# Kernel optimization log

Measured on AMD Instinct MI355X. Metric: run time of the kernel, lower is better.

Reference implementation:

```python
import jax, jax.numpy as jnp
import numpy as np

N = 100000
E = 3200000
H = 4        # heads
C = 8        # hidden_dim per head
G = 512      # number of graphs
F_IN = 128
NEG_SLOPE = 0.2


def glorot(key, shape):
    fan = shape[0] + shape[-1]
    lim = jnp.sqrt(6.0 / fan)
    return jax.random.uniform(key, shape, jnp.float32, -lim, lim)


def setup_inputs() -> dict:
    key = jax.random.key(0)
    ks = jax.random.split(key, 32)
    x = jax.random.normal(ks[0], (N, F_IN), jnp.float32)
    edge_index = jax.random.randint(ks[1], (2, E), 0, N, jnp.int64)
    batch = jnp.sort(jax.random.randint(ks[2], (N,), 0, G, jnp.int64))
    d = {"x": x, "edge_index": edge_index, "batch": batch}
    in_dims = [F_IN, H * C, H * C, H * C]
    for i, din in enumerate(in_dims, start=1):
        d[f"W{i}"] = glorot(ks[3 + 4 * i], (din, H * C))
        d[f"as{i}"] = glorot(ks[4 + 4 * i], (H, C))
        d[f"ad{i}"] = glorot(ks[5 + 4 * i], (H, C))
        d[f"b{i}"] = jnp.zeros((H * C,), jnp.float32)
    d["fc_w"] = glorot(ks[30], (H * C, 1))
    d["fc_b"] = jnp.zeros((1,), jnp.float32)
    return d


def gat_layer(x, src, dst, W, a_src, a_dst, b):
    # x: [N, din]; src/dst: [E'] (with self-loops); returns [N, H*C]
    h = (x @ W).reshape(N, H, C)                         # [N,H,C]
    al_s = jnp.einsum('nhc,hc->nh', h, a_src)            # [N,H]
    al_d = jnp.einsum('nhc,hc->nh', h, a_dst)
    e = jax.nn.leaky_relu(al_s[src] + al_d[dst], NEG_SLOPE)  # [E',H]
    m = jax.ops.segment_max(e, dst, num_segments=N)      # [N,H]
    ee = jnp.exp(e - m[dst])
    denom = jax.ops.segment_sum(ee, dst, num_segments=N) # [N,H]
    alpha = ee / denom[dst]
    msg = alpha[:, :, None] * h[src]                     # [E',H,C]
    out = jax.ops.segment_sum(msg, dst, num_segments=N)  # [N,H,C]
    return out.reshape(N, H * C) + b


def reference(x, edge_index, batch, W1, as1, ad1, b1, W2, as2, ad2, b2,
              W3, as3, ad3, b3, W4, as4, ad4, b4, fc_w, fc_b):
    # PyG GATConv default: add self-loops
    loop = jnp.arange(N, dtype=edge_index.dtype)
    src = jnp.concatenate([edge_index[0], loop])
    dst = jnp.concatenate([edge_index[1], loop])
    h = jax.nn.elu(gat_layer(x, src, dst, W1, as1, ad1, b1))
    h = jax.nn.elu(gat_layer(h, src, dst, W2, as2, ad2, b2))
    h = jax.nn.elu(gat_layer(h, src, dst, W3, as3, ad3, b3))
    h = jax.nn.elu(gat_layer(h, src, dst, W4, as4, ad4, b4))
    # global mean pool over graphs
    sums = jax.ops.segment_sum(h, batch, num_segments=G)          # [G,HC]
    cnts = jax.ops.segment_sum(jnp.ones((N,), h.dtype), batch, num_segments=G)
    pooled = sums / jnp.maximum(cnts, 1.0)[:, None]
    return pooled @ fc_w + fc_b                                   # [G,1]
```

## Files before the change

### kernel.cpp

```cpp
#include <hip/hip_runtime.h>
#include <hip/hip_fp16.h>
#include <math.h>

#define NN 100000
#define NE 3200000
#define NHEAD 4
#define HC 32
#define NG 512
#define EDGES (NE + NN)

#define G1BLKS (NN / 8)

#define BKT_BITS 9
#define BKT_SIZE 512
#define NBKT 196
#define CHUNK1 16384
#define NB1 ((EDGES + CHUNK1 - 1) / CHUNK1)
#define NB1S 204
#define CAP2 18432
#define NBIN2 2048
#define PCHUNK 128

__device__ __forceinline__ float lrelu(float x) { return x > 0.f ? x : 0.2f * x; }
__device__ __forceinline__ int src_quarter(int src) {
    return (src >= 50000) ? ((src >= 75000) ? 3 : 2) : ((src >= 25000) ? 1 : 0);
}

__global__ __launch_bounds__(256) void gemm1(
    const float* __restrict__ x, const float* __restrict__ W1,
    const float* __restrict__ as1, const float* __restrict__ ad1,
    __half* __restrict__ h, float* __restrict__ als, float* __restrict__ ald) {
    __shared__ float Wl[128 * HC];
    __shared__ float xl[8][128];
    int tid = threadIdx.x;
    for (int i = tid; i < 128 * HC; i += 256) Wl[i] = W1[i];
    int n0 = blockIdx.x * 8;
    {
        float4 v = *reinterpret_cast<const float4*>(x + n0 * 128 + tid * 4);
        int idx = tid * 4;
        int r = idx >> 7, c = idx & 127;
        *reinterpret_cast<float4*>(&xl[r][c]) = v;
    }
    __syncthreads();
    int r = tid >> 5, col = tid & 31;
    int n = n0 + r;
    float acc = 0.f;
#pragma unroll
    for (int k = 0; k < 128; ++k) acc = fmaf(xl[r][k], Wl[k * HC + col], acc);
    float s = acc * as1[col];
    float d = acc * ad1[col];
#pragma unroll
    for (int off = 1; off < 8; off <<= 1) {
        s += __shfl_xor(s, off);
        d += __shfl_xor(d, off);
    }
    h[n * HC + col] = __float2half(acc);
    if ((col & 7) == 0) {
        als[n * NHEAD + (col >> 3)] = s;
        ald[n * NHEAD + (col >> 3)] = d;
    }
}

__global__ __launch_bounds__(512) void pass1_hist(const int* __restrict__ ei,
                                                  int* __restrict__ CmatT) {
    __shared__ int hcnt[NBKT];
    for (int i = threadIdx.x; i < NBKT; i += 512) hcnt[i] = 0;
    __syncthreads();
    int base = blockIdx.x * CHUNK1;
    int lim = min(base + CHUNK1, EDGES);
    for (int e = base + threadIdx.x; e < lim; e += 512) {
        int dst = (e < NE) ? ei[NE + e] : (e - NE);
        atomicAdd(&hcnt[dst >> BKT_BITS], 1);
    }
    __syncthreads();
    for (int i = threadIdx.x; i < NBKT; i += 512)
        CmatT[i * NB1S + blockIdx.x] = hcnt[i];
}

__global__ __launch_bounds__(64) void colscan2(int* __restrict__ CmatT,
                                               int* __restrict__ degTot) {
    int k = blockIdx.x;
    int lane = threadIdx.x;
    int* p = CmatT + k * NB1S;
    int i0 = lane * 4;
    int v0 = (i0 + 0 < NB1) ? p[i0 + 0] : 0;
    int v1 = (i0 + 1 < NB1) ? p[i0 + 1] : 0;
    int v2 = (i0 + 2 < NB1) ? p[i0 + 2] : 0;
    int v3 = (i0 + 3 < NB1) ? p[i0 + 3] : 0;
    int e1 = v0, e2 = v0 + v1, e3 = v0 + v1 + v2;
    int tot = e3 + v3;
    int run = tot;
#pragma unroll
    for (int off = 1; off < 64; off <<= 1) {
        int u = __shfl_up(run, off);
        if (lane >= off) run += u;
    }
    int excl = run - tot;
    if (i0 + 0 < NB1) p[i0 + 0] = excl;
    if (i0 + 1 < NB1) p[i0 + 1] = excl + e1;
    if (i0 + 2 < NB1) p[i0 + 2] = excl + e2;
    if (i0 + 3 < NB1) p[i0 + 3] = excl + e3;
    if (lane == 63) degTot[k] = run;
}

__global__ __launch_bounds__(256) void bucket_apex(const int* __restrict__ degTot,
                                                   int* __restrict__ bucketStart) {
    __shared__ int tot[256];
    int k = threadIdx.x;
    int own = (k < NBKT) ? degTot[k] : 0;
    tot[k] = own;
    __syncthreads();
    for (int off = 1; off < 256; off <<= 1) {
        int u = (k >= off) ? tot[k - off] : 0;
        __syncthreads();
        tot[k] += u;
        __syncthreads();
    }
    if (k < NBKT) bucketStart[k] = tot[k] - own;
    if (k == 255) bucketStart[NBKT] = tot[255];
}

__global__ __launch_bounds__(512) void pass1_scatter(const int* __restrict__ ei,
                                                     const int* __restrict__ CmatT,
                                                     const int* __restrict__ bucketStart,
                                                     unsigned int* __restrict__ ebuf) {
    __shared__ int cur[NBKT];
    for (int i = threadIdx.x; i < NBKT; i += 512)
        cur[i] = bucketStart[i] + CmatT[i * NB1S + blockIdx.x];
    __syncthreads();
    int base = blockIdx.x * CHUNK1;
    int lim = min(base + CHUNK1, EDGES);
    for (int e = base + threadIdx.x; e < lim; e += 512) {
        int src, dst;
        if (e < NE) { src = ei[e]; dst = ei[NE + e]; }
        else        { src = dst = e - NE; }
        int pos = atomicAdd(&cur[dst >> BKT_BITS], 1);
        ebuf[pos] = ((unsigned int)(dst & (BKT_SIZE - 1)) << 20) | (unsigned int)src;
    }
}

__global__ __launch_bounds__(1024) void pass2_sort(const unsigned int* __restrict__ ebuf,
                                                   const int* __restrict__ bucketStart,
                                                   int* __restrict__ csrsrc,
                                                   int* __restrict__ rowst) {
    __shared__ int hist[NBIN2];
    __shared__ int pairs[1024];
    __shared__ int staging[CAP2];
    int t = threadIdx.x;
    int k = blockIdx.x;
    int start = bucketStart[k], end = bucketStart[k + 1];
    int count = end - start;
    hist[t] = 0;
    hist[t + 1024] = 0;
    __syncthreads();
    for (int i = start + t; i < end; i += 1024) {
        unsigned int v = ebuf[i];
        int src = (int)(v & 0xFFFFFu);
        atomicAdd(&hist[(int)((v >> 20) << 2) | src_quarter(src)], 1);
    }
    __syncthreads();
    int h0 = hist[2 * t], h1 = hist[2 * t + 1];
    pairs[t] = h0 + h1;
    __syncthreads();
    for (int off = 1; off < 1024; off <<= 1) {
        int u = (t >= off) ? pairs[t - off] : 0;
        __syncthreads();
        pairs[t] += u;
        __syncthreads();
    }
    int e0 = pairs[t] - h0 - h1;
    int e1 = e0 + h0;
    __syncthreads();
    hist[2 * t] = e0;
    hist[2 * t + 1] = e1;
    if ((t & 1) == 0) rowst[k * BKT_SIZE + (t >> 1)] = start + e0;
    __syncthreads();
    for (int i = start + t; i < end; i += 1024) {
        unsigned int v = ebuf[i];
        int src = (int)(v & 0xFFFFFu);
        int pos = atomicAdd(&hist[(int)((v >> 20) << 2) | src_quarter(src)], 1);
        if (pos < CAP2) staging[pos] = src;
    }
    __syncthreads();
    for (int i = t; i < count; i += 1024) csrsrc[start + i] = staging[i];
}

template<bool FUSE>
__global__ __launch_bounds__(256) void agg_layer(
    const int* __restrict__ rowst, const int* __restrict__ csrsrc,
    const float* __restrict__ als, const float* __restrict__ ald,
    const __half* __restrict__ h, const float* __restrict__ bias,
    const float* __restrict__ Wn, const float* __restrict__ asn,
    const float* __restrict__ adn,
    __half* __restrict__ h_out, float* __restrict__ als_out,
    float* __restrict__ ald_out, float* __restrict__ act_out) {
    __shared__ float Wl[HC * HC];
    int tid = threadIdx.x;
    if (FUSE) {
        for (int i = tid; i < HC * HC; i += 256) Wl[i] = Wn[i];
        __syncthreads();
    }
    int g = blockIdx.x * 8 + (tid >> 5);
    int lane = tid & 31;
    int head = lane >> 3;
    int slot = lane & 7;
    float adh = ald[g * NHEAD + head];
    int beg = rowst[g], end = rowst[g + 1];

    float acc[8];
#pragma unroll
    for (int j = 0; j < 8; ++j) acc[j] = 0.f;
    float dsum = 0.f;
    const __half* hL = h + lane;

    for (int c0 = beg; c0 < end; c0 += 16) {
        int eA = c0 + slot;
        int eB = eA + 8;
        int sA = (eA < end) ? __builtin_nontemporal_load(csrsrc + eA) : 0;
        int sB = (eB < end) ? __builtin_nontemporal_load(csrsrc + eB) : 0;
        float pA = __expf(lrelu(als[sA * NHEAD + head] + adh));
        float pB = __expf(lrelu(als[sB * NHEAD + head] + adh));
        pA = (eA < end) ? pA : 0.f;
        pB = (eB < end) ? pB : 0.f;
        dsum += pA + pB;
        int sjA[8], sjB[8];
#pragma unroll
        for (int j = 0; j < 8; ++j) {
            sjA[j] = __shfl(sA, j, 32);
            sjB[j] = __shfl(sB, j, 32);
        }
        __half hvA[8], hvB[8];
#pragma unroll
        for (int j = 0; j < 8; ++j) hvA[j] = hL[sjA[j] * HC];
#pragma unroll
        for (int j = 0; j < 8; ++j) hvB[j] = hL[sjB[j] * HC];
#pragma unroll
        for (int j = 0; j < 8; ++j)
            acc[j] = fmaf(__shfl(pA, (head << 3) | j, 32), __half2float(hvA[j]), acc[j]);
#pragma unroll
        for (int j = 0; j < 8; ++j)
            acc[j] = fmaf(__shfl(pB, (head << 3) | j, 32), __half2float(hvB[j]), acc[j]);
    }
    float a = ((acc[0] + acc[1]) + (acc[2] + acc[3])) +
              ((acc[4] + acc[5]) + (acc[6] + acc[7]));
    dsum += __shfl_xor(dsum, 1, 32);
    dsum += __shfl_xor(dsum, 2, 32);
    dsum += __shfl_xor(dsum, 4, 32);

    float v = a / dsum + bias[lane];
    float av = v > 0.f ? v : (__expf(v) - 1.f);
    if (!FUSE) {
        act_out[g * HC + lane] = av;
        return;
    }
    float hacc = 0.f;
#pragma unroll
    for (int kk = 0; kk < HC; ++kk)
        hacc = fmaf(__shfl(av, kk, 32), Wl[kk * HC + lane], hacc);
    h_out[g * HC + lane] = __float2half(hacc);
    float sv = hacc * asn[lane];
    float dv = hacc * adn[lane];
#pragma unroll
    for (int off = 1; off < 8; off <<= 1) {
        sv += __shfl_xor(sv, off);
        dv += __shfl_xor(dv, off);
    }
    if ((lane & 7) == 0) {
        als_out[g * NHEAD + head] = sv;
        ald_out[g * NHEAD + head] = dv;
    }
}

__global__ void pool_init(float* __restrict__ sums, float* __restrict__ cnt) {
    int i = blockIdx.x * blockDim.x + threadIdx.x;
    if (i < NG * HC) sums[i] = 0.f;
    if (i < NG) cnt[i] = 0.f;
}

__global__ __launch_bounds__(256) void pool_seg(const float* __restrict__ act,
                                                const int* __restrict__ batch,
                                                float* __restrict__ sums,
                                                float* __restrict__ cnt) {
    int grp = blockIdx.x * 8 + (threadIdx.x >> 5);
    int lane = threadIdx.x & 31;
    int n0 = grp * PCHUNK;
    if (n0 >= NN) return;
    int n1 = min(n0 + PCHUNK, NN);
    int curg = batch[n0];
    float acc = 0.f, c = 0.f;
    for (int n = n0; n < n1; ++n) {
        int gg = batch[n];
        if (gg != curg) {
            atomicAdd(&sums[curg * HC + lane], acc);
            if (lane == 0) atomicAdd(&cnt[curg], c);
            acc = 0.f; c = 0.f; curg = gg;
        }
        acc += act[n * HC + lane];
        c += 1.f;
    }
    atomicAdd(&sums[curg * HC + lane], acc);
    if (lane == 0) atomicAdd(&cnt[curg], c);
}

__global__ void fc_out(const float* __restrict__ sums, const float* __restrict__ cnt,
                       const float* __restrict__ fcw, const float* __restrict__ fcb,
                       float* __restrict__ out) {
    int g = blockIdx.x;
    int lane = threadIdx.x;
    float v = (lane < HC) ? sums[g * HC + lane] * fcw[lane] : 0.f;
#pragma unroll
    for (int off = 32; off; off >>= 1) v += __shfl_down(v, off);
    if (lane == 0) out[g] = v / fmaxf(cnt[g], 1.f) + fcb[0];
}

extern "C" void kernel_launch(void* const* d_in, const int* in_sizes, int n_in,
                              void* d_out, int out_size, void* d_ws, size_t ws_size,
                              hipStream_t stream) {
    const float* x     = (const float*)d_in[0];
    const int*   ei    = (const int*)d_in[1];
    const int*   batch = (const int*)d_in[2];
    const float* W[4]   = {(const float*)d_in[3],  (const float*)d_in[7],
                           (const float*)d_in[11], (const float*)d_in[15]};
    const float* asr[4] = {(const float*)d_in[4],  (const float*)d_in[8],
                           (const float*)d_in[12], (const float*)d_in[16]};
    const float* adt[4] = {(const float*)d_in[5],  (const float*)d_in[9],
                           (const float*)d_in[13], (const float*)d_in[17]};
    const float* bb[4]  = {(const float*)d_in[6],  (const float*)d_in[10],
                           (const float*)d_in[14], (const float*)d_in[18]};
    const float* fcw = (const float*)d_in[19];
    const float* fcb = (const float*)d_in[20];
    float* out = (float*)d_out;

    char* ws = (char*)d_ws;
    size_t off = 0;
    auto carve = [&](size_t bytes) {
        void* p = ws + off;
        off += (bytes + 255) & ~size_t(255);
        return p;
    };
    __half* hA   = (__half*)carve(sizeof(__half) * NN * HC);
    __half* hB   = (__half*)carve(sizeof(__half) * NN * HC);
    float* actF  = (float*)carve(sizeof(float) * NN * HC);
    float* alsA  = (float*)carve(sizeof(float) * NN * NHEAD);
    float* aldA  = (float*)carve(sizeof(float) * NN * NHEAD);
    float* alsB  = (float*)carve(sizeof(float) * NN * NHEAD);
    float* aldB  = (float*)carve(sizeof(float) * NN * NHEAD);
    int*   CmatT = (int*)carve(sizeof(int) * NBKT * NB1S);
    int*   degTot= (int*)carve(sizeof(int) * NBKT);
    int*   bkst  = (int*)carve(sizeof(int) * (NBKT + 1));
    unsigned int* ebuf = (unsigned int*)carve(sizeof(unsigned int) * EDGES);
    int*   rowst = (int*)carve(sizeof(int) * NBKT * BKT_SIZE);
    int*   csrsrc= (int*)carve(sizeof(int) * EDGES);
    float* sums  = (float*)carve(sizeof(float) * NG * HC);
    float* cnt   = (float*)carve(sizeof(float) * NG);

    pass1_hist<<<NB1, 512, 0, stream>>>(ei, CmatT);
    colscan2<<<NBKT, 64, 0, stream>>>(CmatT, degTot);
    bucket_apex<<<1, 256, 0, stream>>>(degTot, bkst);
    pass1_scatter<<<NB1, 512, 0, stream>>>(ei, CmatT, bkst, ebuf);
    pass2_sort<<<NBKT, 1024, 0, stream>>>(ebuf, bkst, csrsrc, rowst);

    gemm1<<<G1BLKS, 256, 0, stream>>>(x, W[0], asr[0], adt[0], hA, alsA, aldA);

    agg_layer<true><<<G1BLKS, 256, 0, stream>>>(rowst, csrsrc, alsA, aldA, hA, bb[0],
                                                W[1], asr[1], adt[1],
                                                hB, alsB, aldB, nullptr);
    agg_layer<true><<<G1BLKS, 256, 0, stream>>>(rowst, csrsrc, alsB, aldB, hB, bb[1],
                                                W[2], asr[2], adt[2],
                                                hA, alsA, aldA, nullptr);
    agg_layer<true><<<G1BLKS, 256, 0, stream>>>(rowst, csrsrc, alsA, aldA, hA, bb[2],
                                                W[3], asr[3], adt[3],
                                                hB, alsB, aldB, nullptr);
    agg_layer<false><<<G1BLKS, 256, 0, stream>>>(rowst, csrsrc, alsB, aldB, hB, bb[3],
                                                 nullptr, nullptr, nullptr,
                                                 nullptr, nullptr, nullptr, actF);

    pool_init<<<(NG * HC + 255) / 256, 256, 0, stream>>>(sums, cnt);
    pool_seg<<<((NN + PCHUNK - 1) / PCHUNK + 7) / 8, 256, 0, stream>>>(actF, batch,
                                                                       sums, cnt);
    fc_out<<<NG, 64, 0, stream>>>(sums, cnt, fcw, fcb, out);
}
```

Measured before the change: 473.0 us.

## Split aggregation into four source-quarter passes for cache locality

Each node's CSR row is split into four sub-ranges by source quarter, which the sort already orders by. Aggregation runs as four launches per layer, each gathering only from one quarter of the feature table, so the gathered working set is smaller and more likely to stay in cache. Partial numerators and denominators go through global scratch buffers between launches. The cost is extra launches, extra global reads and writes of the partials, and a loop unrolled over 8 edges instead of 16.

```diff
diff --git a/kernel.cpp b/kernel.cpp
--- a/kernel.cpp
+++ b/kernel.cpp
@@ -142,7 +142,7 @@
 __global__ __launch_bounds__(1024) void pass2_sort(const unsigned int* __restrict__ ebuf,
                                                    const int* __restrict__ bucketStart,
                                                    int* __restrict__ csrsrc,
-                                                   int* __restrict__ rowst) {
+                                                   int* __restrict__ rowst4) {
     __shared__ int hist[NBIN2];
     __shared__ int pairs[1024];
     __shared__ int staging[CAP2];
@@ -173,7 +173,8 @@
     __syncthreads();
     hist[2 * t] = e0;
     hist[2 * t + 1] = e1;
-    if ((t & 1) == 0) rowst[k * BKT_SIZE + (t >> 1)] = start + e0;
+    rowst4[(k << 11) | (2 * t)]     = start + e0;
+    rowst4[(k << 11) | (2 * t + 1)] = start + e1;
     __syncthreads();
     for (int i = start + t; i < end; i += 1024) {
         unsigned int v = ebuf[i];
@@ -185,11 +186,13 @@
     for (int i = t; i < count; i += 1024) csrsrc[start + i] = staging[i];
 }
 
-template<bool FUSE>
-__global__ __launch_bounds__(256) void agg_layer(
-    const int* __restrict__ rowst, const int* __restrict__ csrsrc,
+template<int PHASE, bool FUSE>
+__global__ __launch_bounds__(256) void agg_q(
+    const int* __restrict__ rowst4, const int* __restrict__ csrsrc,
     const float* __restrict__ als, const float* __restrict__ ald,
-    const __half* __restrict__ h, const float* __restrict__ bias,
+    const __half* __restrict__ h, int q,
+    float* __restrict__ accP, float* __restrict__ dsumP,
+    const float* __restrict__ bias,
     const float* __restrict__ Wn, const float* __restrict__ asn,
     const float* __restrict__ adn,
     __half* __restrict__ h_out, float* __restrict__ als_out,
@@ -205,7 +208,7 @@
     int head = lane >> 3;
     int slot = lane & 7;
     float adh = ald[g * NHEAD + head];
-    int beg = rowst[g], end = rowst[g + 1];
+    int beg = rowst4[g * 4 + q], end = rowst4[g * 4 + q + 1];
 
     float acc[8];
 #pragma unroll
@@ -213,33 +216,18 @@
     float dsum = 0.f;
     const __half* hL = h + lane;
 
-    for (int c0 = beg; c0 < end; c0 += 16) {
-        int eA = c0 + slot;
-        int eB = eA + 8;
-        int sA = (eA < end) ? __builtin_nontemporal_load(csrsrc + eA) : 0;
-        int sB = (eB < end) ? __builtin_nontemporal_load(csrsrc + eB) : 0;
-        float pA = __expf(lrelu(als[sA * NHEAD + head] + adh));
-        float pB = __expf(lrelu(als[sB * NHEAD + head] + adh));
-        pA = (eA < end) ? pA : 0.f;
-        pB = (eB < end) ? pB : 0.f;
-        dsum += pA + pB;
-        int sjA[8], sjB[8];
+    for (int c0 = beg; c0 < end; c0 += 8) {
+        int e = c0 + slot;
+        int s = (e < end) ? __builtin_nontemporal_load(csrsrc + e) : 0;
+        float p = __expf(lrelu(als[s * NHEAD + head] + adh));
+        p = (e < end) ? p : 0.f;
+        dsum += p;
 #pragma unroll
         for (int j = 0; j < 8; ++j) {
-            sjA[j] = __shfl(sA, j, 32);
-            sjB[j] = __shfl(sB, j, 32);
+            float pj = __shfl(p, (head << 3) | j, 32);
+            int sj = __shfl(s, j, 32);
+            acc[j] = fmaf(pj, __half2float(hL[sj * HC]), acc[j]);
         }
-        __half hvA[8], hvB[8];
-#pragma unroll
-        for (int j = 0; j < 8; ++j) hvA[j] = hL[sjA[j] * HC];
-#pragma unroll
-        for (int j = 0; j < 8; ++j) hvB[j] = hL[sjB[j] * HC];
-#pragma unroll
-        for (int j = 0; j < 8; ++j)
-            acc[j] = fmaf(__shfl(pA, (head << 3) | j, 32), __half2float(hvA[j]), acc[j]);
-#pragma unroll
-        for (int j = 0; j < 8; ++j)
-            acc[j] = fmaf(__shfl(pB, (head << 3) | j, 32), __half2float(hvB[j]), acc[j]);
     }
     float a = ((acc[0] + acc[1]) + (acc[2] + acc[3])) +
               ((acc[4] + acc[5]) + (acc[6] + acc[7]));
@@ -247,6 +235,23 @@
     dsum += __shfl_xor(dsum, 2, 32);
     dsum += __shfl_xor(dsum, 4, 32);
 
+    if (PHASE == 0) {
+        __builtin_nontemporal_store(a, accP + g * HC + lane);
+        if (slot == 0)
+            __builtin_nontemporal_store(dsum, dsumP + g * NHEAD + head);
+        return;
+    }
+    if (PHASE == 1) {
+        float pa = __builtin_nontemporal_load(accP + g * HC + lane);
+        __builtin_nontemporal_store(a + pa, accP + g * HC + lane);
+        if (slot == 0) {
+            float pd = __builtin_nontemporal_load(dsumP + g * NHEAD + head);
+            __builtin_nontemporal_store(dsum + pd, dsumP + g * NHEAD + head);
+        }
+        return;
+    }
+    a += __builtin_nontemporal_load(accP + g * HC + lane);
+    dsum += __builtin_nontemporal_load(dsumP + g * NHEAD + head);
     float v = a / dsum + bias[lane];
     float av = v > 0.f ? v : (__expf(v) - 1.f);
     if (!FUSE) {
@@ -341,6 +346,8 @@
     __half* hA   = (__half*)carve(sizeof(__half) * NN * HC);
     __half* hB   = (__half*)carve(sizeof(__half) * NN * HC);
     float* actF  = (float*)carve(sizeof(float) * NN * HC);
+    float* accP  = (float*)carve(sizeof(float) * NN * HC);
+    float* dsumP = (float*)carve(sizeof(float) * NN * NHEAD);
     float* alsA  = (float*)carve(sizeof(float) * NN * NHEAD);
     float* aldA  = (float*)carve(sizeof(float) * NN * NHEAD);
     float* alsB  = (float*)carve(sizeof(float) * NN * NHEAD);
@@ -349,7 +356,7 @@
     int*   degTot= (int*)carve(sizeof(int) * NBKT);
     int*   bkst  = (int*)carve(sizeof(int) * (NBKT + 1));
     unsigned int* ebuf = (unsigned int*)carve(sizeof(unsigned int) * EDGES);
-    int*   rowst = (int*)carve(sizeof(int) * NBKT * BKT_SIZE);
+    int*   rowst4= (int*)carve(sizeof(int) * NBKT * NBIN2);
     int*   csrsrc= (int*)carve(sizeof(int) * EDGES);
     float* sums  = (float*)carve(sizeof(float) * NG * HC);
     float* cnt   = (float*)carve(sizeof(float) * NG);
@@ -358,22 +365,37 @@
     colscan2<<<NBKT, 64, 0, stream>>>(CmatT, degTot);
     bucket_apex<<<1, 256, 0, stream>>>(degTot, bkst);
     pass1_scatter<<<NB1, 512, 0, stream>>>(ei, CmatT, bkst, ebuf);
-    pass2_sort<<<NBKT, 1024, 0, stream>>>(ebuf, bkst, csrsrc, rowst);
+    pass2_sort<<<NBKT, 1024, 0, stream>>>(ebuf, bkst, csrsrc, rowst4);
 
     gemm1<<<G1BLKS, 256, 0, stream>>>(x, W[0], asr[0], adt[0], hA, alsA, aldA);
 
-    agg_layer<true><<<G1BLKS, 256, 0, stream>>>(rowst, csrsrc, alsA, aldA, hA, bb[0],
-                                                W[1], asr[1], adt[1],
-                                                hB, alsB, aldB, nullptr);
-    agg_layer<true><<<G1BLKS, 256, 0, stream>>>(rowst, csrsrc, alsB, aldB, hB, bb[1],
-                                                W[2], asr[2], adt[2],
-                                                hA, alsA, aldA, nullptr);
-    agg_layer<true><<<G1BLKS, 256, 0, stream>>>(rowst, csrsrc, alsA, aldA, hA, bb[2],
-                                                W[3], asr[3], adt[3],
-                                                hB, alsB, aldB, nullptr);
-    agg_layer<false><<<G1BLKS, 256, 0, stream>>>(rowst, csrsrc, alsB, aldB, hB, bb[3],
-                                                 nullptr, nullptr, nullptr,
-                                                 nullptr, nullptr, nullptr, actF);
+    const __half* hIn[4]  = {hA, hB, hA, hB};
+    __half* hOut[4]       = {hB, hA, hB, nullptr};
+    const float* alsIn[4] = {alsA, alsB, alsA, alsB};
+    const float* aldIn[4] = {aldA, aldB, aldA, aldB};
+    float* alsOut[4]      = {alsB, alsA, alsB, nullptr};
+    float* aldOut[4]      = {aldB, aldA, aldB, nullptr};
+    for (int L = 0; L < 4; ++L) {
+        agg_q<0, false><<<G1BLKS, 256, 0, stream>>>(
+            rowst4, csrsrc, alsIn[L], aldIn[L], hIn[L], 0, accP, dsumP,
+            nullptr, nullptr, nullptr, nullptr, nullptr, nullptr, nullptr, nullptr);
+        agg_q<1, false><<<G1BLKS, 256, 0, stream>>>(
+            rowst4, csrsrc, alsIn[L], aldIn[L], hIn[L], 1, accP, dsumP,
+            nullptr, nullptr, nullptr, nullptr, nullptr, nullptr, nullptr, nullptr);
+        agg_q<1, false><<<G1BLKS, 256, 0, stream>>>(
+            rowst4, csrsrc, alsIn[L], aldIn[L], hIn[L], 2, accP, dsumP,
+            nullptr, nullptr, nullptr, nullptr, nullptr, nullptr, nullptr, nullptr);
+        if (L < 3)
+            agg_q<2, true><<<G1BLKS, 256, 0, stream>>>(
+                rowst4, csrsrc, alsIn[L], aldIn[L], hIn[L], 3, accP, dsumP,
+                bb[L], W[L + 1], asr[L + 1], adt[L + 1],
+                hOut[L], alsOut[L], aldOut[L], nullptr);
+        else
+            agg_q<2, false><<<G1BLKS, 256, 0, stream>>>(
+                rowst4, csrsrc, alsIn[L], aldIn[L], hIn[L], 3, accP, dsumP,
+                bb[3], nullptr, nullptr, nullptr,
+                nullptr, nullptr, nullptr, actF);
+    }
 
     pool_init<<<(NG * HC + 255) / 256, 256, 0, stream>>>(sums, cnt);
     pool_seg<<<((NN + PCHUNK - 1) / PCHUNK + 7) / 8, 256, 0, stream>>>(actF, batch,
```

Result: slower. 687.2 us (+45.3%).
